# Performance work log

Measured on AMD Instinct MI355X. Metric: run time of the kernel, lower is better.

## Reference

```python
import jax, jax.numpy as jnp
import numpy as np

LEVELS = 16
FEATURES = 2
HASHMAP_SIZE = 524288
BASE_RES = 16
PER_LEVEL_SCALE = 1.3819

_P1, _P2, _P3 = np.uint32(73856093), np.uint32(19349663), np.uint32(83492791)
# 8 trilinear corner offsets, bit order (x, y, z)
_OFFSETS = np.array([[ox, oy, oz] for ox in (0, 1) for oy in (0, 1) for oz in (0, 1)], dtype=np.int32)


def setup_inputs() -> dict:
    key = jax.random.key(0)
    kx, kt = jax.random.split(key)
    x = jax.random.uniform(kx, (2000000, 3), dtype=jnp.float32)
    tables = jax.random.normal(kt, (LEVELS, HASHMAP_SIZE, FEATURES), dtype=jnp.float32) * 0.01
    return {"x": x, "tables": tables}


def _hash_coords(corners_u32):
    # corners_u32: [N, 8, 3] uint32; spatial hash with uint32 wraparound.
    h = (corners_u32[..., 0] * _P1) ^ (corners_u32[..., 1] * _P2) ^ (corners_u32[..., 2] * _P3)
    return (h % np.uint32(HASHMAP_SIZE)).astype(jnp.int32)  # [N, 8]


def _encode(x, tables):
    offsets_i = jnp.asarray(_OFFSETS)                 # [8, 3] int32
    offsets_f = offsets_i.astype(x.dtype)             # [8, 3]
    embeds = []
    for l in range(LEVELS):
        res = int(BASE_RES * PER_LEVEL_SCALE ** l)
        pos = x * res                                  # [N, 3]
        pos_floor = jnp.floor(pos)
        w = pos - pos_floor                            # [N, 3] trilinear weights
        base = pos_floor.astype(jnp.int32)             # non-negative (x in [0,1])
        corners = (base[:, None, :] + offsets_i).astype(jnp.uint32)  # [N, 8, 3]
        idx = _hash_coords(corners)                    # [N, 8]
        vals = tables[l][idx]                          # [N, 8, F] gather
        # weight per corner = prod over axes of (w if offset else 1-w)
        wgt = jnp.prod(offsets_f * w[:, None, :] + (1.0 - offsets_f) * (1.0 - w[:, None, :]), axis=-1)  # [N, 8]
        embeds.append(jnp.einsum('nc,ncf->nf', wgt, vals))  # [N, F]
    return jnp.concatenate(embeds, axis=-1)           # [N, LEVELS*F]


def reference(x, tables):
    return _encode(x, tables)
```

## Files before the change

kernel.cpp:

```cpp
#include <hip/hip_runtime.h>
#include <hip/hip_fp16.h>
#include <stdint.h>

#define LEVELS 16
#define FEAT 2
#define TABLE_SIZE 524288
#define TMASK (TABLE_SIZE - 1)

typedef float f32x2 __attribute__((ext_vector_type(2)));
typedef float f32x4 __attribute__((ext_vector_type(4)));
typedef float f32x4u __attribute__((ext_vector_type(4), aligned(8)));

__device__ __constant__ int kRes[LEVELS] = {
    16, 22, 30, 42, 58, 80, 111, 153, 212, 294, 406, 561, 775, 1072, 1481, 2047
};

#define P1 73856093u
#define P2 19349663u
#define P3 83492791u

#define NQ 7
#define HASH0 7
#define NHASH (LEVELS - HASH0)
#define NSTAGE (LEVELS - 5)
#define NFIN 5

constexpr int   cQD[NQ]     = { 17, 23, 31, 43, 59, 81, 112 };
constexpr float cQRes[NQ]   = { 16.0f, 22.0f, 30.0f, 42.0f, 58.0f, 80.0f, 111.0f };
constexpr int   cQCum[NQ+1] = { 0, 4913, 17080, 46871, 126378, 331757, 863198, 2268126 };
#define NCELLS 2268126

__global__ __launch_bounds__(256) void remap1_kernel(
    const float* __restrict__ tables,
    f32x2* __restrict__ dense)
{
    const int d = blockIdx.x * 256 + threadIdx.x;
    if (d >= NCELLS) return;
    int l = 0;
#pragma unroll
    for (int k = 1; k < NQ; ++k)
        if (d >= cQCum[k]) l = k;
    const int D   = cQD[l];
    const int rel = d - cQCum[l];
    const uint32_t bx = rel / (D * D);
    const uint32_t r  = rel - bx * (D * D);
    const uint32_t by = r / D;
    const uint32_t bz = r - by * D;
    const uint32_t slot = ((bx * P1) ^ (by * P2) ^ (bz * P3)) & TMASK;
    const f32x2* __restrict__ tab = reinterpret_cast<const f32x2*>(tables) + (size_t)l * TABLE_SIZE;
    dense[d] = tab[slot];
}

__global__ __launch_bounds__(256) void remap2_kernel(
    const f32x2* __restrict__ dense,
    uint4* __restrict__ qtab)
{
    const int d = blockIdx.x * 256 + threadIdx.x;
    if (d >= NCELLS) return;
    int l = 0;
#pragma unroll
    for (int k = 1; k < NQ; ++k)
        if (d >= cQCum[k]) l = k;
    const int D   = cQD[l];
    const int rel = d - cQCum[l];

    const f32x2* __restrict__ dl = dense + cQCum[l];
    const f32x4u a = *reinterpret_cast<const f32x4u*>(dl + rel);
    const f32x4u b = *reinterpret_cast<const f32x4u*>(dl + rel + D);

    union { __half2 h; uint32_t u; } p0, p1, p2, p3;
    p0.h = __float22half2_rn(make_float2(a.x, a.y));
    p1.h = __float22half2_rn(make_float2(a.z, a.w));
    p2.h = __float22half2_rn(make_float2(b.x, b.y));
    p3.h = __float22half2_rn(make_float2(b.z, b.w));
    qtab[d] = make_uint4(p0.u, p1.u, p2.u, p3.u);
}

__global__ __launch_bounds__(256) void encode_level_kernel(
    const float* __restrict__ x,
    const float* __restrict__ tables,
    f32x2* __restrict__ ws,
    int n, int nb, int l0)
{
    const int l   = l0 + blockIdx.x / nb;
    const int blk = blockIdx.x - (l - l0) * nb;
    const int t   = threadIdx.x;
    const int p0  = blk * 512;

    __shared__ float sx[512 * 3];
    const long long total3 = (long long)n * 3;
    const long long gbase  = (long long)p0 * 3;
#pragma unroll
    for (int k = 0; k < 6; ++k) {
        long long g = gbase + k * 256 + t;
        sx[k * 256 + t] = (g < total3) ? __builtin_nontemporal_load(x + g) : 0.0f;
    }
    __syncthreads();

    const float resf = (float)kRes[l];
    const f32x2* __restrict__ tab = reinterpret_cast<const f32x2*>(tables) + (size_t)l * TABLE_SIZE;

    uint32_t idx[2][8];
    float    wgt[2][8];
#pragma unroll
    for (int s = 0; s < 2; ++s) {
        const int tp = s * 256 + t;
        const float fx = sx[3 * tp + 0] * resf;
        const float fy = sx[3 * tp + 1] * resf;
        const float fz = sx[3 * tp + 2] * resf;
        const float flx = floorf(fx), fly = floorf(fy), flz = floorf(fz);
        const float wx = fx - flx, wy = fy - fly, wz = fz - flz;
        const float ux = 1.0f - wx, uy = 1.0f - wy, uz = 1.0f - wz;
        const uint32_t hx0 = (uint32_t)(int)flx * P1, hx1 = hx0 + P1;
        const uint32_t hy0 = (uint32_t)(int)fly * P2, hy1 = hy0 + P2;
        const uint32_t hz0 = (uint32_t)(int)flz * P3, hz1 = hz0 + P3;
#pragma unroll
        for (int c = 0; c < 8; ++c) {
            const uint32_t hx = (c & 4) ? hx1 : hx0;
            const uint32_t hy = (c & 2) ? hy1 : hy0;
            const uint32_t hz = (c & 1) ? hz1 : hz0;
            idx[s][c] = (hx ^ hy ^ hz) & TMASK;
            wgt[s][c] = ((c & 4) ? wx : ux) * ((c & 2) ? wy : uy) * ((c & 1) ? wz : uz);
        }
    }

    f32x2 v[2][8];
#pragma unroll
    for (int s = 0; s < 2; ++s)
#pragma unroll
        for (int c = 0; c < 8; ++c)
            v[s][c] = tab[idx[s][c]];

#pragma unroll
    for (int s = 0; s < 2; ++s) {
        float f0 = 0.0f, f1 = 0.0f;
#pragma unroll
        for (int c = 0; c < 8; ++c) {
            f0 = fmaf(wgt[s][c], v[s][c].x, f0);
            f1 = fmaf(wgt[s][c], v[s][c].y, f1);
        }
        const int i = p0 + s * 256 + t;
        if (i < n) {
            f32x2 r; r.x = f0; r.y = f1;
            __builtin_nontemporal_store(r, ws + (size_t)(l - 5) * n + i);
        }
    }
}

__global__ __launch_bounds__(256) void encode_dense56_kernel(
    const float* __restrict__ x,
    const uint4* __restrict__ qtab,
    f32x2* __restrict__ ws,
    int n, int nb)
{
    const int lsel = blockIdx.x / nb;
    const int blk  = blockIdx.x - lsel * nb;
    const int t    = threadIdx.x;
    const int p0   = blk * 512;

    __shared__ float sx[512 * 3];
    const long long total3 = (long long)n * 3;
    const long long gbase  = (long long)p0 * 3;
#pragma unroll
    for (int k = 0; k < 6; ++k) {
        long long g = gbase + k * 256 + t;
        sx[k * 256 + t] = (g < total3) ? __builtin_nontemporal_load(x + g) : 0.0f;
    }
    __syncthreads();

    const int   D    = lsel ? 112 : 81;
    const int   DD   = D * D;
    const float resf = lsel ? 111.0f : 80.0f;
    const uint4* __restrict__ qt = qtab + (lsel ? cQCum[6] : cQCum[5]);

    int   q0a[2];
    float wxa[2], wya[2], wza[2];
#pragma unroll
    for (int s = 0; s < 2; ++s) {
        const int tp = s * 256 + t;
        const float fx = sx[3 * tp + 0] * resf;
        const float fy = sx[3 * tp + 1] * resf;
        const float fz = sx[3 * tp + 2] * resf;
        const float flx = floorf(fx), fly = floorf(fy), flz = floorf(fz);
        wxa[s] = fx - flx; wya[s] = fy - fly; wza[s] = fz - flz;
        q0a[s] = ((int)flx * D + (int)fly) * D + (int)flz;
    }

    uint4 A[2], B[2];
#pragma unroll
    for (int s = 0; s < 2; ++s) {
        A[s] = qt[q0a[s]];
        B[s] = qt[q0a[s] + DD];
    }

#pragma unroll
    for (int s = 0; s < 2; ++s) {
        const float wx = wxa[s], wy = wya[s], wz = wza[s];
        const float ux = 1.0f - wx, uy = 1.0f - wy, uz = 1.0f - wz;

        union { uint32_t u; __half2 hh; } c;
        float2 a00, a01, a10, a11, b00, b01, b10, b11;
        c.u = A[s].x; a00 = __half22float2(c.hh);
        c.u = A[s].y; a01 = __half22float2(c.hh);
        c.u = A[s].z; a10 = __half22float2(c.hh);
        c.u = A[s].w; a11 = __half22float2(c.hh);
        c.u = B[s].x; b00 = __half22float2(c.hh);
        c.u = B[s].y; b01 = __half22float2(c.hh);
        c.u = B[s].z; b10 = __half22float2(c.hh);
        c.u = B[s].w; b11 = __half22float2(c.hh);

        const float ya0 = fmaf(uz, a00.x, wz * a01.x), ya1 = fmaf(uz, a10.x, wz * a11.x);
        const float yb0 = fmaf(uz, b00.x, wz * b01.x), yb1 = fmaf(uz, b10.x, wz * b11.x);
        const float f0  = fmaf(ux, fmaf(uy, ya0, wy * ya1), wx * fmaf(uy, yb0, wy * yb1));
        const float za0 = fmaf(uz, a00.y, wz * a01.y), za1 = fmaf(uz, a10.y, wz * a11.y);
        const float zb0 = fmaf(uz, b00.y, wz * b01.y), zb1 = fmaf(uz, b10.y, wz * b11.y);
        const float f1  = fmaf(ux, fmaf(uy, za0, wy * za1), wx * fmaf(uy, zb0, wy * zb1));

        const int i = p0 + s * 256 + t;
        if (i < n) {
            f32x2 r; r.x = f0; r.y = f1;
            __builtin_nontemporal_store(r, ws + (size_t)lsel * n + i);
        }
    }
}

__global__ __launch_bounds__(256) void finalize_kernel(
    const float* __restrict__ x,
    const uint4* __restrict__ qtab,
    const f32x2* __restrict__ ws,
    float* __restrict__ out,
    int n)
{
    __shared__ float s[256 * 33];
    __shared__ float sx[256 * 3];
    const int t  = threadIdx.x;
    const int p0 = blockIdx.x * 256;
    const int m  = min(256, n - p0);

    const long long total3 = (long long)n * 3;
    const long long gbase  = (long long)p0 * 3;
#pragma unroll
    for (int k = 0; k < 3; ++k) {
        long long g = gbase + k * 256 + t;
        sx[k * 256 + t] = (g < total3) ? __builtin_nontemporal_load(x + g) : 0.0f;
    }
    __syncthreads();

    if (t < m) {
        const int i = p0 + t;

        f32x2 h[NSTAGE];
#pragma unroll
        for (int j = 0; j < NSTAGE; ++j)
            h[j] = __builtin_nontemporal_load(ws + (size_t)j * n + i);

        const float px = sx[3 * t + 0];
        const float py = sx[3 * t + 1];
        const float pz = sx[3 * t + 2];

#pragma unroll
        for (int l = 0; l < NFIN; ++l) {
            const int   D    = cQD[l];
            const int   DD   = D * D;
            const float resf = cQRes[l];
            const uint4* __restrict__ qt = qtab + cQCum[l];

            const float fx = px * resf, fy = py * resf, fz = pz * resf;
            const float flx = floorf(fx), fly = floorf(fy), flz = floorf(fz);
            const float wx = fx - flx, wy = fy - fly, wz = fz - flz;
            const float ux = 1.0f - wx, uy = 1.0f - wy, uz = 1.0f - wz;
            const int q0 = (((int)flx * D + (int)fly) * D + (int)flz);

            const uint4 A = qt[q0];
            const uint4 B = qt[q0 + DD];

            union { uint32_t u; __half2 hh; } c;
            float2 a00, a01, a10, a11, b00, b01, b10, b11;
            c.u = A.x; a00 = __half22float2(c.hh);
            c.u = A.y; a01 = __half22float2(c.hh);
            c.u = A.z; a10 = __half22float2(c.hh);
            c.u = A.w; a11 = __half22float2(c.hh);
            c.u = B.x; b00 = __half22float2(c.hh);
            c.u = B.y; b01 = __half22float2(c.hh);
            c.u = B.z; b10 = __half22float2(c.hh);
            c.u = B.w; b11 = __half22float2(c.hh);

            const float ya0 = fmaf(uz, a00.x, wz * a01.x), ya1 = fmaf(uz, a10.x, wz * a11.x);
            const float yb0 = fmaf(uz, b00.x, wz * b01.x), yb1 = fmaf(uz, b10.x, wz * b11.x);
            const float f0  = fmaf(ux, fmaf(uy, ya0, wy * ya1), wx * fmaf(uy, yb0, wy * yb1));
            const float za0 = fmaf(uz, a00.y, wz * a01.y), za1 = fmaf(uz, a10.y, wz * a11.y);
            const float zb0 = fmaf(uz, b00.y, wz * b01.y), zb1 = fmaf(uz, b10.y, wz * b11.y);
            const float f1  = fmaf(ux, fmaf(uy, za0, wy * za1), wx * fmaf(uy, zb0, wy * zb1));

            s[t * 33 + 2 * l + 0] = f0;
            s[t * 33 + 2 * l + 1] = f1;
        }
#pragma unroll
        for (int j = 0; j < NSTAGE; ++j) {
            s[t * 33 + 2 * (NFIN + j) + 0] = h[j].x;
            s[t * 33 + 2 * (NFIN + j) + 1] = h[j].y;
        }
    }
    __syncthreads();

    const int nchunk = m * 8;
    f32x4* __restrict__ o4 = reinterpret_cast<f32x4*>(out) + (size_t)p0 * 8;
#pragma unroll
    for (int j = 0; j < 8; ++j) {
        const int cl = j * 256 + t;
        if (cl < nchunk) {
            const int p = cl >> 3, ch = cl & 7;
            f32x4 q;
            q.x = s[p * 33 + ch * 4 + 0];
            q.y = s[p * 33 + ch * 4 + 1];
            q.z = s[p * 33 + ch * 4 + 2];
            q.w = s[p * 33 + ch * 4 + 3];
            __builtin_nontemporal_store(q, o4 + cl);
        }
    }
}

__global__ __launch_bounds__(256) void hashgrid_enc_kernel(
    const float* __restrict__ x,
    const float* __restrict__ tables,
    float* __restrict__ out,
    int n)
{
    __shared__ float sx[256 * 3];
    const int t = threadIdx.x;
    const int block0 = blockIdx.x * 256;
    const long long total3 = (long long)n * 3;
    const long long gbase = (long long)block0 * 3;
#pragma unroll
    for (int k = 0; k < 3; ++k) {
        long long g = gbase + k * 256 + t;
        sx[k * 256 + t] = (g < total3) ? x[g] : 0.0f;
    }
    __syncthreads();
    const int i = block0 + t;
    if (i >= n) return;
    const float px = sx[3 * t + 0];
    const float py = sx[3 * t + 1];
    const float pz = sx[3 * t + 2];
    float outv[2 * LEVELS];
#pragma unroll
    for (int l = 0; l < LEVELS; ++l) {
        const float resf = (float)kRes[l];
        const float fx = px * resf, fy = py * resf, fz = pz * resf;
        const float flx = floorf(fx), fly = floorf(fy), flz = floorf(fz);
        const float wx = fx - flx, wy = fy - fly, wz = fz - flz;
        const float ux = 1.0f - wx, uy = 1.0f - wy, uz = 1.0f - wz;
        const uint32_t hx0 = (uint32_t)(int)flx * P1, hx1 = hx0 + P1;
        const uint32_t hy0 = (uint32_t)(int)fly * P2, hy1 = hy0 + P2;
        const uint32_t hz0 = (uint32_t)(int)flz * P3, hz1 = hz0 + P3;
        const float* __restrict__ tab = tables + (size_t)l * (TABLE_SIZE * FEAT);
        float f0 = 0.0f, f1 = 0.0f;
#pragma unroll
        for (int c = 0; c < 8; ++c) {
            const uint32_t hx = (c & 4) ? hx1 : hx0;
            const uint32_t hy = (c & 2) ? hy1 : hy0;
            const uint32_t hz = (c & 1) ? hz1 : hz0;
            const uint32_t idx = (hx ^ hy ^ hz) & TMASK;
            const float2 v = *reinterpret_cast<const float2*>(tab + (size_t)idx * FEAT);
            const float w = ((c & 4) ? wx : ux) * ((c & 2) ? wy : uy) * ((c & 1) ? wz : uz);
            f0 = fmaf(w, v.x, f0);
            f1 = fmaf(w, v.y, f1);
        }
        outv[2 * l + 0] = f0;
        outv[2 * l + 1] = f1;
    }
    float4* __restrict__ o4 = reinterpret_cast<float4*>(out + (size_t)i * (2 * LEVELS));
#pragma unroll
    for (int k = 0; k < 8; ++k) {
        o4[k] = make_float4(outv[4 * k + 0], outv[4 * k + 1],
                            outv[4 * k + 2], outv[4 * k + 3]);
    }
}

extern "C" void kernel_launch(void* const* d_in, const int* in_sizes, int n_in,
                              void* d_out, int out_size, void* d_ws, size_t ws_size,
                              hipStream_t stream) {
    const float* x = (const float*)d_in[0];
    const float* tables = (const float*)d_in[1];
    float* out = (float*)d_out;
    const int n = in_sizes[0] / 3;

    const size_t stag_b = (size_t)NSTAGE * (size_t)n * sizeof(f32x2);
    const size_t s1_b   = ((size_t)NCELLS + 256) * sizeof(f32x2);
    const size_t r0_b   = (stag_b > s1_b ? stag_b : s1_b);
    const size_t qoff   = (r0_b + 15) & ~(size_t)15;
    const size_t need   = qoff + (size_t)NCELLS * sizeof(uint4);

    if (ws_size >= need) {
        f32x2* staging = (f32x2*)d_ws;
        f32x2* stage1  = (f32x2*)d_ws;
        uint4* qtab    = (uint4*)((char*)d_ws + qoff);

        const int nbcell = (NCELLS + 255) / 256;
        hipLaunchKernelGGL(remap1_kernel, dim3(nbcell), dim3(256), 0, stream, tables, stage1);
        hipLaunchKernelGGL(remap2_kernel, dim3(nbcell), dim3(256), 0, stream, stage1, qtab);

        const int nb512 = (n + 511) / 512;
        hipLaunchKernelGGL(encode_level_kernel, dim3(nb512 * NHASH), dim3(256), 0, stream,
                           x, tables, staging, n, nb512, HASH0);
        hipLaunchKernelGGL(encode_dense56_kernel, dim3(nb512 * 2), dim3(256), 0, stream,
                           x, qtab, staging, n, nb512);

        const int nb256 = (n + 255) / 256;
        hipLaunchKernelGGL(finalize_kernel, dim3(nb256), dim3(256), 0, stream,
                           x, qtab, staging, out, n);
    } else {
        const int nb = (n + 255) / 256;
        hipLaunchKernelGGL(hashgrid_enc_kernel, dim3(nb), dim3(256), 0, stream,
                           x, tables, out, n);
    }
}
```

Measured before the change: 970.9 us.

## Merge hash and dense encode kernels and stage intermediates as fp16

```diff
diff --git a/kernel.cpp b/kernel.cpp
--- a/kernel.cpp
+++ b/kernel.cpp
@@ -20,8 +20,7 @@
 #define P3 83492791u
 
 #define NQ 7
-#define HASH0 7
-#define NHASH (LEVELS - HASH0)
+#define NHASH 9
 #define NSTAGE (LEVELS - 5)
 #define NFIN 5
 
@@ -76,16 +75,17 @@
     qtab[d] = make_uint4(p0.u, p1.u, p2.u, p3.u);
 }
 
-__global__ __launch_bounds__(256) void encode_level_kernel(
+__global__ __launch_bounds__(256) void encode_merged_kernel(
     const float* __restrict__ x,
     const float* __restrict__ tables,
-    f32x2* __restrict__ ws,
-    int n, int nb, int l0)
+    const uint4* __restrict__ qtab,
+    uint32_t* __restrict__ ws,
+    int n, int nb)
 {
-    const int l   = l0 + blockIdx.x / nb;
-    const int blk = blockIdx.x - (l - l0) * nb;
-    const int t   = threadIdx.x;
-    const int p0  = blk * 512;
+    const int role = blockIdx.x / nb;
+    const int blk  = blockIdx.x - role * nb;
+    const int t    = threadIdx.x;
+    const int p0   = blk * 512;
 
     __shared__ float sx[512 * 3];
     const long long total3 = (long long)n * 3;
@@ -97,129 +97,113 @@
     }
     __syncthreads();
 
-    const float resf = (float)kRes[l];
-    const f32x2* __restrict__ tab = reinterpret_cast<const f32x2*>(tables) + (size_t)l * TABLE_SIZE;
-
-    uint32_t idx[2][8];
-    float    wgt[2][8];
-#pragma unroll
-    for (int s = 0; s < 2; ++s) {
-        const int tp = s * 256 + t;
-        const float fx = sx[3 * tp + 0] * resf;
-        const float fy = sx[3 * tp + 1] * resf;
-        const float fz = sx[3 * tp + 2] * resf;
-        const float flx = floorf(fx), fly = floorf(fy), flz = floorf(fz);
-        const float wx = fx - flx, wy = fy - fly, wz = fz - flz;
-        const float ux = 1.0f - wx, uy = 1.0f - wy, uz = 1.0f - wz;
-        const uint32_t hx0 = (uint32_t)(int)flx * P1, hx1 = hx0 + P1;
-        const uint32_t hy0 = (uint32_t)(int)fly * P2, hy1 = hy0 + P2;
-        const uint32_t hz0 = (uint32_t)(int)flz * P3, hz1 = hz0 + P3;
-#pragma unroll
-        for (int c = 0; c < 8; ++c) {
-            const uint32_t hx = (c & 4) ? hx1 : hx0;
-            const uint32_t hy = (c & 2) ? hy1 : hy0;
-            const uint32_t hz = (c & 1) ? hz1 : hz0;
-            idx[s][c] = (hx ^ hy ^ hz) & TMASK;
-            wgt[s][c] = ((c & 4) ? wx : ux) * ((c & 2) ? wy : uy) * ((c & 1) ? wz : uz);
-        }
-    }
-
-    f32x2 v[2][8];
-#pragma unroll
-    for (int s = 0; s < 2; ++s)
-#pragma unroll
-        for (int c = 0; c < 8; ++c)
-            v[s][c] = tab[idx[s][c]];
-
-#pragma unroll
-    for (int s = 0; s < 2; ++s) {
-        float f0 = 0.0f, f1 = 0.0f;
-#pragma unroll
-        for (int c = 0; c < 8; ++c) {
-            f0 = fmaf(wgt[s][c], v[s][c].x, f0);
-            f1 = fmaf(wgt[s][c], v[s][c].y, f1);
-        }
-        const int i = p0 + s * 256 + t;
-        if (i < n) {
-            f32x2 r; r.x = f0; r.y = f1;
-            __builtin_nontemporal_store(r, ws + (size_t)(l - 5) * n + i);
-        }
-    }
-}
-
-__global__ __launch_bounds__(256) void encode_dense56_kernel(
-    const float* __restrict__ x,
-    const uint4* __restrict__ qtab,
-    f32x2* __restrict__ ws,
-    int n, int nb)
-{
-    const int lsel = blockIdx.x / nb;
-    const int blk  = blockIdx.x - lsel * nb;
-    const int t    = threadIdx.x;
-    const int p0   = blk * 512;
-
-    __shared__ float sx[512 * 3];
-    const long long total3 = (long long)n * 3;
-    const long long gbase  = (long long)p0 * 3;
-#pragma unroll
-    for (int k = 0; k < 6; ++k) {
-        long long g = gbase + k * 256 + t;
-        sx[k * 256 + t] = (g < total3) ? __builtin_nontemporal_load(x + g) : 0.0f;
-    }
-    __syncthreads();
-
-    const int   D    = lsel ? 112 : 81;
-    const int   DD   = D * D;
-    const float resf = lsel ? 111.0f : 80.0f;
-    const uint4* __restrict__ qt = qtab + (lsel ? cQCum[6] : cQCum[5]);
-
-    int   q0a[2];
-    float wxa[2], wya[2], wza[2];
-#pragma unroll
-    for (int s = 0; s < 2; ++s) {
-        const int tp = s * 256 + t;
-        const float fx = sx[3 * tp + 0] * resf;
-        const float fy = sx[3 * tp + 1] * resf;
-        const float fz = sx[3 * tp + 2] * resf;
-        const float flx = floorf(fx), fly = floorf(fy), flz = floorf(fz);
-        wxa[s] = fx - flx; wya[s] = fy - fly; wza[s] = fz - flz;
-        q0a[s] = ((int)flx * D + (int)fly) * D + (int)flz;
-    }
-
-    uint4 A[2], B[2];
-#pragma unroll
-    for (int s = 0; s < 2; ++s) {
-        A[s] = qt[q0a[s]];
-        B[s] = qt[q0a[s] + DD];
-    }
-
-#pragma unroll
-    for (int s = 0; s < 2; ++s) {
-        const float wx = wxa[s], wy = wya[s], wz = wza[s];
-        const float ux = 1.0f - wx, uy = 1.0f - wy, uz = 1.0f - wz;
-
-        union { uint32_t u; __half2 hh; } c;
-        float2 a00, a01, a10, a11, b00, b01, b10, b11;
-        c.u = A[s].x; a00 = __half22float2(c.hh);
-        c.u = A[s].y; a01 = __half22float2(c.hh);
-        c.u = A[s].z; a10 = __half22float2(c.hh);
-        c.u = A[s].w; a11 = __half22float2(c.hh);
-        c.u = B[s].x; b00 = __half22float2(c.hh);
-        c.u = B[s].y; b01 = __half22float2(c.hh);
-        c.u = B[s].z; b10 = __half22float2(c.hh);
-        c.u = B[s].w; b11 = __half22float2(c.hh);
-
-        const float ya0 = fmaf(uz, a00.x, wz * a01.x), ya1 = fmaf(uz, a10.x, wz * a11.x);
-        const float yb0 = fmaf(uz, b00.x, wz * b01.x), yb1 = fmaf(uz, b10.x, wz * b11.x);
-        const float f0  = fmaf(ux, fmaf(uy, ya0, wy * ya1), wx * fmaf(uy, yb0, wy * yb1));
-        const float za0 = fmaf(uz, a00.y, wz * a01.y), za1 = fmaf(uz, a10.y, wz * a11.y);
-        const float zb0 = fmaf(uz, b00.y, wz * b01.y), zb1 = fmaf(uz, b10.y, wz * b11.y);
-        const float f1  = fmaf(ux, fmaf(uy, za0, wy * za1), wx * fmaf(uy, zb0, wy * zb1));
-
-        const int i = p0 + s * 256 + t;
-        if (i < n) {
-            f32x2 r; r.x = f0; r.y = f1;
-            __builtin_nontemporal_store(r, ws + (size_t)lsel * n + i);
+    if (role < NHASH) {
+        const int l = 7 + role;
+        const float resf = (float)kRes[l];
+        const f32x2* __restrict__ tab = reinterpret_cast<const f32x2*>(tables) + (size_t)l * TABLE_SIZE;
+
+        uint32_t idx[2][8];
+        float    wgt[2][8];
+#pragma unroll
+        for (int s = 0; s < 2; ++s) {
+            const int tp = s * 256 + t;
+            const float fx = sx[3 * tp + 0] * resf;
+            const float fy = sx[3 * tp + 1] * resf;
+            const float fz = sx[3 * tp + 2] * resf;
+            const float flx = floorf(fx), fly = floorf(fy), flz = floorf(fz);
+            const float wx = fx - flx, wy = fy - fly, wz = fz - flz;
+            const float ux = 1.0f - wx, uy = 1.0f - wy, uz = 1.0f - wz;
+            const uint32_t hx0 = (uint32_t)(int)flx * P1, hx1 = hx0 + P1;
+            const uint32_t hy0 = (uint32_t)(int)fly * P2, hy1 = hy0 + P2;
+            const uint32_t hz0 = (uint32_t)(int)flz * P3, hz1 = hz0 + P3;
+#pragma unroll
+            for (int c = 0; c < 8; ++c) {
+                const uint32_t hx = (c & 4) ? hx1 : hx0;
+                const uint32_t hy = (c & 2) ? hy1 : hy0;
+                const uint32_t hz = (c & 1) ? hz1 : hz0;
+                idx[s][c] = (hx ^ hy ^ hz) & TMASK;
+                wgt[s][c] = ((c & 4) ? wx : ux) * ((c & 2) ? wy : uy) * ((c & 1) ? wz : uz);
+            }
+        }
+
+        f32x2 v[2][8];
+#pragma unroll
+        for (int s = 0; s < 2; ++s)
+#pragma unroll
+            for (int c = 0; c < 8; ++c)
+                v[s][c] = tab[idx[s][c]];
+
+#pragma unroll
+        for (int s = 0; s < 2; ++s) {
+            float f0 = 0.0f, f1 = 0.0f;
+#pragma unroll
+            for (int c = 0; c < 8; ++c) {
+                f0 = fmaf(wgt[s][c], v[s][c].x, f0);
+                f1 = fmaf(wgt[s][c], v[s][c].y, f1);
+            }
+            const int i = p0 + s * 256 + t;
+            if (i < n) {
+                union { __half2 h; uint32_t u; } r;
+                r.h = __floats2half2_rn(f0, f1);
+                __builtin_nontemporal_store(r.u, ws + (size_t)(l - 5) * n + i);
+            }
+        }
+    } else {
+        const int lsel = role - NHASH;
+        const int   D    = lsel ? 112 : 81;
+        const int   DD   = D * D;
+        const float resf = lsel ? 111.0f : 80.0f;
+        const uint4* __restrict__ qt = qtab + (lsel ? cQCum[6] : cQCum[5]);
+
+        int   q0a[2];
+        float wxa[2], wya[2], wza[2];
+#pragma unroll
+        for (int s = 0; s < 2; ++s) {
+            const int tp = s * 256 + t;
+            const float fx = sx[3 * tp + 0] * resf;
+            const float fy = sx[3 * tp + 1] * resf;
+            const float fz = sx[3 * tp + 2] * resf;
+            const float flx = floorf(fx), fly = floorf(fy), flz = floorf(fz);
+            wxa[s] = fx - flx; wya[s] = fy - fly; wza[s] = fz - flz;
+            q0a[s] = ((int)flx * D + (int)fly) * D + (int)flz;
+        }
+
+        uint4 A[2], B[2];
+#pragma unroll
+        for (int s = 0; s < 2; ++s) {
+            A[s] = qt[q0a[s]];
+            B[s] = qt[q0a[s] + DD];
+        }
+
+#pragma unroll
+        for (int s = 0; s < 2; ++s) {
+            const float wx = wxa[s], wy = wya[s], wz = wza[s];
+            const float ux = 1.0f - wx, uy = 1.0f - wy, uz = 1.0f - wz;
+
+            union { uint32_t u; __half2 hh; } c;
+            float2 a00, a01, a10, a11, b00, b01, b10, b11;
+            c.u = A[s].x; a00 = __half22float2(c.hh);
+            c.u = A[s].y; a01 = __half22float2(c.hh);
+            c.u = A[s].z; a10 = __half22float2(c.hh);
+            c.u = A[s].w; a11 = __half22float2(c.hh);
+            c.u = B[s].x; b00 = __half22float2(c.hh);
+            c.u = B[s].y; b01 = __half22float2(c.hh);
+            c.u = B[s].z; b10 = __half22float2(c.hh);
+            c.u = B[s].w; b11 = __half22float2(c.hh);
+
+            const float ya0 = fmaf(uz, a00.x, wz * a01.x), ya1 = fmaf(uz, a10.x, wz * a11.x);
+            const float yb0 = fmaf(uz, b00.x, wz * b01.x), yb1 = fmaf(uz, b10.x, wz * b11.x);
+            const float f0  = fmaf(ux, fmaf(uy, ya0, wy * ya1), wx * fmaf(uy, yb0, wy * yb1));
+            const float za0 = fmaf(uz, a00.y, wz * a01.y), za1 = fmaf(uz, a10.y, wz * a11.y);
+            const float zb0 = fmaf(uz, b00.y, wz * b01.y), zb1 = fmaf(uz, b10.y, wz * b11.y);
+            const float f1  = fmaf(ux, fmaf(uy, za0, wy * za1), wx * fmaf(uy, zb0, wy * zb1));
+
+            const int i = p0 + s * 256 + t;
+            if (i < n) {
+                union { __half2 h; uint32_t u; } r;
+                r.h = __floats2half2_rn(f0, f1);
+                __builtin_nontemporal_store(r.u, ws + (size_t)lsel * n + i);
+            }
         }
     }
 }
@@ -227,7 +211,7 @@
 __global__ __launch_bounds__(256) void finalize_kernel(
     const float* __restrict__ x,
     const uint4* __restrict__ qtab,
-    const f32x2* __restrict__ ws,
+    const uint32_t* __restrict__ ws,
     float* __restrict__ out,
     int n)
 {
@@ -249,7 +233,7 @@
     if (t < m) {
         const int i = p0 + t;
 
-        f32x2 h[NSTAGE];
+        uint32_t h[NSTAGE];
 #pragma unroll
         for (int j = 0; j < NSTAGE; ++j)
             h[j] = __builtin_nontemporal_load(ws + (size_t)j * n + i);
@@ -297,8 +281,11 @@
         }
 #pragma unroll
         for (int j = 0; j < NSTAGE; ++j) {
-            s[t * 33 + 2 * (NFIN + j) + 0] = h[j].x;
-            s[t * 33 + 2 * (NFIN + j) + 1] = h[j].y;
+            union { uint32_t u; __half2 hh; } c;
+            c.u = h[j];
+            const float2 hv = __half22float2(c.hh);
+            s[t * 33 + 2 * (NFIN + j) + 0] = hv.x;
+            s[t * 33 + 2 * (NFIN + j) + 1] = hv.y;
         }
     }
     __syncthreads();
@@ -385,26 +372,24 @@
     float* out = (float*)d_out;
     const int n = in_sizes[0] / 3;
 
-    const size_t stag_b = (size_t)NSTAGE * (size_t)n * sizeof(f32x2);
+    const size_t stag_b = (size_t)NSTAGE * (size_t)n * sizeof(uint32_t);
     const size_t s1_b   = ((size_t)NCELLS + 256) * sizeof(f32x2);
     const size_t r0_b   = (stag_b > s1_b ? stag_b : s1_b);
     const size_t qoff   = (r0_b + 15) & ~(size_t)15;
     const size_t need   = qoff + (size_t)NCELLS * sizeof(uint4);
 
     if (ws_size >= need) {
-        f32x2* staging = (f32x2*)d_ws;
-        f32x2* stage1  = (f32x2*)d_ws;
-        uint4* qtab    = (uint4*)((char*)d_ws + qoff);
+        uint32_t* staging = (uint32_t*)d_ws;
+        f32x2*    stage1  = (f32x2*)d_ws;
+        uint4*    qtab    = (uint4*)((char*)d_ws + qoff);
 
         const int nbcell = (NCELLS + 255) / 256;
         hipLaunchKernelGGL(remap1_kernel, dim3(nbcell), dim3(256), 0, stream, tables, stage1);
         hipLaunchKernelGGL(remap2_kernel, dim3(nbcell), dim3(256), 0, stream, stage1, qtab);
 
         const int nb512 = (n + 511) / 512;
-        hipLaunchKernelGGL(encode_level_kernel, dim3(nb512 * NHASH), dim3(256), 0, stream,
-                           x, tables, staging, n, nb512, HASH0);
-        hipLaunchKernelGGL(encode_dense56_kernel, dim3(nb512 * 2), dim3(256), 0, stream,
-                           x, qtab, staging, n, nb512);
+        hipLaunchKernelGGL(encode_merged_kernel, dim3(nb512 * (NHASH + 2)), dim3(256), 0, stream,
+                           x, tables, qtab, staging, n, nb512);
 
         const int nb256 = (n + 255) / 256;
         hipLaunchKernelGGL(finalize_kernel, dim3(nb256), dim3(256), 0, stream,
```

Measured after the change: 936.8 us. 1.04x faster.
